# Optimization experiments

Measured on AMD Instinct MI355X. Metric: run time of the kernel, lower is better.

Reference implementation:

```python
import jax, jax.numpy as jnp
import numpy as np

EMB_DIM = 1024
N_HEADS = 16
HEAD_DIM = EMB_DIM // N_HEADS
WINDOW = 128
B, T = 4, 2048


def setup_inputs() -> dict:
    key = jax.random.key(0)
    k1, k2, k3 = jax.random.split(key, 3)
    x = jax.random.normal(k1, (B, T, EMB_DIM), dtype=jnp.float32)
    # nn.Linear weights: stored as [out, in], applied as x @ W^T
    s1 = 1.0 / np.sqrt(EMB_DIM)
    w_qkv = jax.random.uniform(k2, (3 * EMB_DIM, EMB_DIM), jnp.float32, -s1, s1)
    w_out = jax.random.uniform(k3, (EMB_DIM, EMB_DIM), jnp.float32, -s1, s1)
    return {"x": x, "w_qkv": w_qkv, "w_out": w_out}


def reference(x, w_qkv, w_out):
    Bs, Ts, C = x.shape
    scale = HEAD_DIM ** -0.5
    qkv = x @ w_qkv.T                                   # [B,T,3C]
    qkv = qkv.reshape(Bs, Ts, 3, N_HEADS, HEAD_DIM)
    qkv = jnp.transpose(qkv, (2, 0, 3, 1, 4))           # [3,B,H,T,D]
    q, k, v = qkv[0], qkv[1], qkv[2]
    scores = jnp.einsum('bhtd,bhsd->bhts', q, k) * scale  # [B,H,T,T]
    i = jnp.arange(Ts)[:, None]
    j = jnp.arange(Ts)[None, :]
    # causal AND within sliding window: i - WINDOW <= j <= i
    allowed = (j <= i) & (j >= i - WINDOW)               # [T,T] bool
    scores = jnp.where(allowed[None, None], scores, -jnp.inf)
    attn = jax.nn.softmax(scores, axis=-1)
    out = jnp.einsum('bhts,bhsd->bhtd', attn, v)         # [B,H,T,D]
    out = jnp.transpose(out, (0, 2, 1, 3)).reshape(Bs, Ts, C)
    return out @ w_out.T
```

## Files before the change

kernel.cpp:

```cpp
#include <hip/hip_runtime.h>
#include <hip/hip_bf16.h>
#include <stdint.h>

typedef __attribute__((ext_vector_type(8))) short bf16x8;
typedef __attribute__((ext_vector_type(4))) float f32x4;
typedef __attribute__((ext_vector_type(4))) unsigned short u16x4;

#define B_ 4
#define T_ 2048
#define C_ 1024
#define H_ 16
#define D_ 64

__device__ __forceinline__ unsigned short f2bf(float f) {
  union { float f; uint32_t u; } v; v.f = f;
  uint32_t u = v.u;
  uint32_t r = (u + 0x7FFFu + ((u >> 16) & 1u)) >> 16;
  return (unsigned short)r;
}

__global__ void __launch_bounds__(256) cast_all(const float* __restrict__ x,
                                                const float* __restrict__ wqkv,
                                                const float* __restrict__ wout,
                                                unsigned short* __restrict__ xb,
                                                unsigned short* __restrict__ wqkvb,
                                                unsigned short* __restrict__ woutb) {
  int bid = blockIdx.x;
  const float* src; unsigned short* dst; int i;
  if (bid < 8192)       { src = x;    dst = xb;    i = bid * 256 + threadIdx.x; }
  else if (bid < 11264) { src = wqkv; dst = wqkvb; i = (bid - 8192) * 256 + threadIdx.x; }
  else                  { src = wout; dst = woutb; i = (bid - 11264) * 256 + threadIdx.x; }
  float4 f = ((const float4*)src)[i];
  u16x4 o;
  o[0] = f2bf(f.x); o[1] = f2bf(f.y); o[2] = f2bf(f.z); o[3] = f2bf(f.w);
  ((u16x4*)dst)[i] = o;
}

__global__ void __launch_bounds__(256) gemm_qkv(const unsigned short* __restrict__ A,
                                                const unsigned short* __restrict__ Bm,
                                                unsigned short* __restrict__ qb,
                                                unsigned short* __restrict__ kb,
                                                unsigned short* __restrict__ vb) {
  __shared__ short lds[32768];
  const int tid = threadIdx.x;
  const int bm = blockIdx.y * 128;
  const int bn = blockIdx.x * 128;

  const int wave = tid >> 6;
  const int l = tid & 63;
  const int wm = wave >> 1, wn = wave & 1;
  const int lm = l & 15, lq = l >> 4;
  const int lr = l >> 2;
  const int lc = (l & 3) << 3;

  f32x4 acc[4][4];
#pragma unroll
  for (int i = 0; i < 4; i++)
#pragma unroll
    for (int j = 0; j < 4; j++) acc[i][j] = (f32x4){0.f, 0.f, 0.f, 0.f};

  const unsigned short* gsrc[4];
  int ldoff[4];
#pragma unroll
  for (int i = 0; i < 4; i++) {
    int c = wave * 4 + i;
    if (c < 8) {
      gsrc[i] = A + (size_t)(bm + 16 * c + lr) * 1024 + lc;
      ldoff[i] = c * 512;
    } else {
      gsrc[i] = Bm + (size_t)(bn + 16 * (c - 8) + lr) * 1024 + lc;
      ldoff[i] = 16384 + (c - 8) * 512;
    }
  }

#define STAGE(q, kk)                                                             \
  do {                                                                           \
    _Pragma("unroll")                                                            \
    for (int i = 0; i < 4; i++) {                                                \
      __builtin_amdgcn_global_load_lds(                                          \
          (__attribute__((address_space(1))) void*)(uintptr_t)(const void*)(gsrc[i] + (kk)), \
          (__attribute__((address_space(3))) void*)(lds + ldoff[i] + (q) * 4096),            \
          16, 0, 0);                                                             \
    }                                                                            \
  } while (0)

  STAGE(0, 0);
  STAGE(1, 32);
  __syncthreads();

  for (int kk = 0; kk < 1024; kk += 64) {
    const int cp = (kk >> 6) & 1;
    if (kk + 64 < 1024) {
      STAGE(2 * (1 - cp), kk + 64);
      STAGE(2 * (1 - cp) + 1, kk + 96);
    }
#pragma unroll
    for (int sub = 0; sub < 2; sub++) {
      const int q = 2 * cp + sub;
      const short* As_ = lds + q * 4096;
      const short* Bs_ = lds + 16384 + q * 4096;
      bf16x8 af[4], bfr[4];
#pragma unroll
      for (int i = 0; i < 4; i++)
        af[i] = *(const bf16x8*)&As_[(wm * 64 + 16 * i + lm) * 32 + 8 * lq];
#pragma unroll
      for (int j = 0; j < 4; j++)
        bfr[j] = *(const bf16x8*)&Bs_[(wn * 64 + 16 * j + lm) * 32 + 8 * lq];
#pragma unroll
      for (int i = 0; i < 4; i++)
#pragma unroll
        for (int j = 0; j < 4; j++)
          acc[i][j] = __builtin_amdgcn_mfma_f32_16x16x32_bf16(af[i], bfr[j], acc[i][j], 0, 0, 0);
    }
    __syncthreads();
  }
#undef STAGE

  if (bn >= 2048) {
#pragma unroll
    for (int i = 0; i < 4; i++)
#pragma unroll
      for (int j = 0; j < 4; j++) {
        int m0 = bm + wm * 64 + 16 * i + 4 * lq;
        int n = (bn - 2048) + wn * 64 + 16 * j + lm;
        int h = n >> 6, d = n & 63;
        int b = m0 >> 11, t = m0 & 2047;
        u16x4 o;
#pragma unroll
        for (int r = 0; r < 4; r++) o[r] = f2bf(acc[i][j][r]);
        *(u16x4*)&vb[(((size_t)(b * 16 + h)) * 64 + d) * 2048 + t] = o;
      }
  } else {
#pragma unroll
    for (int i = 0; i < 4; i++)
#pragma unroll
      for (int j = 0; j < 4; j++)
#pragma unroll
        for (int r = 0; r < 4; r++)
          lds[(wm * 64 + 16 * i + 4 * lq + r) * 132 + wn * 64 + 16 * j + lm] =
              (short)f2bf(acc[i][j][r]);
    __syncthreads();
#pragma unroll
    for (int k = 0; k < 8; k++) {
      int c = tid + 256 * k;
      int row = c >> 4;
      int col = (c & 15) << 3;
      bf16x8 v = *(const bf16x8*)&lds[row * 132 + col];
      int m = bm + row, n = bn + col;
      int which = n >> 10, rem = n & 1023;
      int h = rem >> 6, d = rem & 63;
      int b = m >> 11, t = m & 2047;
      unsigned short* dst = (which == 0) ? qb : kb;
      *(bf16x8*)&dst[(((size_t)(b * 16 + h)) * 2048 + t) * 64 + d] = v;
    }
  }
}

__global__ void __launch_bounds__(256) gemm_out(const unsigned short* __restrict__ A,
                                                const unsigned short* __restrict__ Bm,
                                                float* __restrict__ fo) {
  __shared__ short lds[32768];
  const int tid = threadIdx.x;
  const int bm = blockIdx.y * 128;
  const int bn = blockIdx.x * 128;
  const int wave = tid >> 6;
  const int l = tid & 63;
  const int wm = wave >> 1, wn = wave & 1;
  const int lm = l & 15, lq = l >> 4;
  const int lr = l >> 2;
  const int lc = (l & 3) << 3;

  f32x4 acc[4][4];
#pragma unroll
  for (int i = 0; i < 4; i++)
#pragma unroll
    for (int j = 0; j < 4; j++) acc[i][j] = (f32x4){0.f, 0.f, 0.f, 0.f};

  const unsigned short* gsrc[4];
  int ldoff[4];
#pragma unroll
  for (int i = 0; i < 4; i++) {
    int c = wave * 4 + i;
    if (c < 8) {
      gsrc[i] = A + (size_t)(bm + 16 * c + lr) * 1024 + lc;
      ldoff[i] = c * 512;
    } else {
      gsrc[i] = Bm + (size_t)(bn + 16 * (c - 8) + lr) * 1024 + lc;
      ldoff[i] = 16384 + (c - 8) * 512;
    }
  }

#define STAGE(q, kk)                                                             \
  do {                                                                           \
    _Pragma("unroll")                                                            \
    for (int i = 0; i < 4; i++) {                                                \
      __builtin_amdgcn_global_load_lds(                                          \
          (__attribute__((address_space(1))) void*)(uintptr_t)(const void*)(gsrc[i] + (kk)), \
          (__attribute__((address_space(3))) void*)(lds + ldoff[i] + (q) * 4096),            \
          16, 0, 0);                                                             \
    }                                                                            \
  } while (0)

  STAGE(0, 0);
  STAGE(1, 32);
  __syncthreads();

  for (int kk = 0; kk < 1024; kk += 64) {
    const int cp = (kk >> 6) & 1;
    if (kk + 64 < 1024) {
      STAGE(2 * (1 - cp), kk + 64);
      STAGE(2 * (1 - cp) + 1, kk + 96);
    }
#pragma unroll
    for (int sub = 0; sub < 2; sub++) {
      const int q = 2 * cp + sub;
      const short* As_ = lds + q * 4096;
      const short* Bs_ = lds + 16384 + q * 4096;
      bf16x8 af[4], bfr[4];
#pragma unroll
      for (int i = 0; i < 4; i++)
        af[i] = *(const bf16x8*)&As_[(wm * 64 + 16 * i + lm) * 32 + 8 * lq];
#pragma unroll
      for (int j = 0; j < 4; j++)
        bfr[j] = *(const bf16x8*)&Bs_[(wn * 64 + 16 * j + lm) * 32 + 8 * lq];
#pragma unroll
      for (int i = 0; i < 4; i++)
#pragma unroll
        for (int j = 0; j < 4; j++)
          acc[i][j] = __builtin_amdgcn_mfma_f32_16x16x32_bf16(af[i], bfr[j], acc[i][j], 0, 0, 0);
    }
    __syncthreads();
  }
#undef STAGE

#pragma unroll
  for (int i = 0; i < 4; i++)
#pragma unroll
    for (int j = 0; j < 4; j++)
#pragma unroll
      for (int r = 0; r < 4; r++) {
        int m = bm + wm * 64 + 16 * i + 4 * lq + r;
        int n = bn + wn * 64 + 16 * j + lm;
        fo[(size_t)m * 1024 + n] = acc[i][j][r];
      }
}

__global__ void __launch_bounds__(256, 4) attn_swa(const unsigned short* __restrict__ Qb,
                                                   const unsigned short* __restrict__ Kb,
                                                   const unsigned short* __restrict__ Vt,
                                                   unsigned short* __restrict__ Ob) {
  __shared__ short P[4][16 * 48];
  const int wv = threadIdx.x >> 6;
  const int l = threadIdx.x & 63;
  const int wid = blockIdx.x * 4 + wv;
  const int bh = wid >> 6;
  const int t0 = (wid & 63) << 5;
  const int lm = l & 15, lq = l >> 4;
  const size_t base = (size_t)bh * (T_ * D_);

  bf16x8 qf[2][2];
#pragma unroll
  for (int qt = 0; qt < 2; qt++) {
    qf[qt][0] = *(const bf16x8*)(Qb + base + (size_t)(t0 + 16 * qt + lm) * 64 + 8 * lq);
    qf[qt][1] = *(const bf16x8*)(Qb + base + (size_t)(t0 + 16 * qt + lm) * 64 + 32 + 8 * lq);
  }

  float mst[2] = {-1e30f, -1e30f}, lst[2] = {0.f, 0.f};
  f32x4 Oa[2][4];
#pragma unroll
  for (int qt = 0; qt < 2; qt++)
#pragma unroll
    for (int jt = 0; jt < 4; jt++) Oa[qt][jt] = (f32x4){0.f, 0.f, 0.f, 0.f};

  const float cs = 0.125f * 1.44269504f;
  int jstart = t0 - 128; if (jstart < 0) jstart = 0;

  for (int j0 = jstart; j0 < t0 + 32; j0 += 32) {
    bf16x8 ka[2][2];
#pragma unroll
    for (int hh = 0; hh < 2; hh++) {
      int kr = j0 + 16 * hh + lm;
      ka[hh][0] = *(const bf16x8*)(Kb + base + (size_t)kr * 64 + 8 * lq);
      ka[hh][1] = *(const bf16x8*)(Kb + base + (size_t)kr * 64 + 32 + 8 * lq);
    }
    bf16x8 vf[4];
#pragma unroll
    for (int jt = 0; jt < 4; jt++)
      vf[jt] = *(const bf16x8*)(Vt + base + (size_t)(16 * jt + lm) * 2048 + j0 + 8 * lq);

#pragma unroll
    for (int qt = 0; qt < 2; qt++) {
      const int t0q = t0 + 16 * qt;
      const int t = t0q + lm;
      f32x4 s0 = (f32x4){0.f, 0.f, 0.f, 0.f}, s1 = (f32x4){0.f, 0.f, 0.f, 0.f};
      s0 = __builtin_amdgcn_mfma_f32_16x16x32_bf16(ka[0][0], qf[qt][0], s0, 0, 0, 0);
      s0 = __builtin_amdgcn_mfma_f32_16x16x32_bf16(ka[0][1], qf[qt][1], s0, 0, 0, 0);
      s1 = __builtin_amdgcn_mfma_f32_16x16x32_bf16(ka[1][0], qf[qt][0], s1, 0, 0, 0);
      s1 = __builtin_amdgcn_mfma_f32_16x16x32_bf16(ka[1][1], qf[qt][1], s1, 0, 0, 0);
      float sv[8];
      float m2 = -1e30f;
#pragma unroll
      for (int hh = 0; hh < 2; hh++)
#pragma unroll
        for (int r = 0; r < 4; r++) {
          int k = j0 + 16 * hh + 4 * lq + r;
          float x = (hh ? s1[r] : s0[r]) * cs;
          bool okm = (k <= t) && (k + 128 >= t);
          sv[hh * 4 + r] = okm ? x : -1e30f;
          m2 = fmaxf(m2, sv[hh * 4 + r]);
        }
      m2 = fmaxf(m2, __shfl_xor(m2, 16));
      m2 = fmaxf(m2, __shfl_xor(m2, 32));
      float mn = fmaxf(mst[qt], m2);
      float a = __builtin_amdgcn_exp2f(mst[qt] - mn);
      float ps = 0.f;
#pragma unroll
      for (int i = 0; i < 8; i++) {
        sv[i] = (sv[i] > -1e29f) ? __builtin_amdgcn_exp2f(sv[i] - mn) : 0.f;
        ps += sv[i];
      }
      ps += __shfl_xor(ps, 16);
      ps += __shfl_xor(ps, 32);
      lst[qt] = lst[qt] * a + ps;
      mst[qt] = mn;
#pragma unroll
      for (int hh = 0; hh < 2; hh++) {
        u16x4 pk;
#pragma unroll
        for (int r = 0; r < 4; r++) pk[r] = f2bf(sv[hh * 4 + r]);
        *(u16x4*)&P[wv][lm * 48 + 16 * hh + 4 * lq] = pk;
      }
      float al[4];
#pragma unroll
      for (int r = 0; r < 4; r++) al[r] = __shfl(a, 4 * lq + r);
#pragma unroll
      for (int jt = 0; jt < 4; jt++)
#pragma unroll
        for (int r = 0; r < 4; r++) Oa[qt][jt][r] *= al[r];
      bf16x8 pa = *(const bf16x8*)&P[wv][lm * 48 + 8 * lq];
#pragma unroll
      for (int jt = 0; jt < 4; jt++)
        Oa[qt][jt] = __builtin_amdgcn_mfma_f32_16x16x32_bf16(pa, vf[jt], Oa[qt][jt], 0, 0, 0);
    }
  }
  const int b = bh >> 4, h = bh & 15;
#pragma unroll
  for (int qt = 0; qt < 2; qt++) {
    float inv = 1.0f / lst[qt];
    float invl[4];
#pragma unroll
    for (int r = 0; r < 4; r++) invl[r] = __shfl(inv, 4 * lq + r);
#pragma unroll
    for (int r = 0; r < 4; r++) {
      int t = t0 + 16 * qt + 4 * lq + r;
#pragma unroll
      for (int jt = 0; jt < 4; jt++) {
        int c = h * 64 + 16 * jt + lm;
        Ob[((size_t)(b * T_ + t)) * 1024 + c] = f2bf(Oa[qt][jt][r] * invl[r]);
      }
    }
  }
}

extern "C" void kernel_launch(void* const* d_in, const int* in_sizes, int n_in,
                              void* d_out, int out_size, void* d_ws, size_t ws_size,
                              hipStream_t stream) {
  const float* x = (const float*)d_in[0];
  const float* w_qkv = (const float*)d_in[1];
  const float* w_out = (const float*)d_in[2];
  float* out = (float*)d_out;

  unsigned short* xb = (unsigned short*)d_ws;
  unsigned short* wqkvb = xb + (size_t)8192 * 1024;
  unsigned short* woutb = wqkvb + (size_t)3072 * 1024;
  unsigned short* qb = woutb + (size_t)1024 * 1024;
  unsigned short* kb = qb + (size_t)64 * 2048 * 64;
  unsigned short* vb = kb + (size_t)64 * 2048 * 64;

  cast_all<<<12288, 256, 0, stream>>>(x, w_qkv, w_out, xb, wqkvb, woutb);

  gemm_qkv<<<dim3(24, 64), 256, 0, stream>>>(xb, wqkvb, qb, kb, vb);

  attn_swa<<<1024, 256, 0, stream>>>(qb, kb, vb, xb);

  gemm_out<<<dim3(8, 64), 256, 0, stream>>>(xb, woutb, out);
}
```

Baseline: 205.0 us.

## Specialize attention mask per KV block and skip lazy softmax rescales

Splits the sliding-window attention KV loop into first/interior/diagonal blocks with template-specialized masks, so interior blocks skip mask evaluation entirely. Adds a lazy-rescale path that keeps the old running max when the new block max is within a threshold, avoiding the output-accumulator rescale and its shuffles. Also swaps the manual bf16 rounding for the HIP intrinsic conversion. The lazy-max path depends on exp2 of bounded values staying in range and adds a wave vote and a branch per step; masked entries now rely on exp2 of a very negative number underflowing to zero.

```diff
diff --git a/kernel.cpp b/kernel.cpp
--- a/kernel.cpp
+++ b/kernel.cpp
@@ -17,6 +17,13 @@
   uint32_t u = v.u;
   uint32_t r = (u + 0x7FFFu + ((u >> 16) & 1u)) >> 16;
   return (unsigned short)r;
+}
+
+__device__ __forceinline__ unsigned short f2bfh(float f) {
+  __hip_bfloat16 h = __float2bfloat16(f);
+  unsigned short u;
+  __builtin_memcpy(&u, &h, 2);
+  return u;
 }
 
 __global__ void __launch_bounds__(256) cast_all(const float* __restrict__ x,
@@ -245,6 +252,73 @@
       }
 }
 
+template <int MODE>
+__device__ __forceinline__ void qt_step(int j0, int t0q, int lm, int lq, short* Pw,
+                                        const bf16x8 (&ka)[2][2], const bf16x8 (&vf)[4],
+                                        bf16x8 qf0, bf16x8 qf1,
+                                        float& mstq, float& lstq, f32x4 (&Oaq)[4]) {
+  const float cs = 0.125f * 1.44269504f;
+  const int t = t0q + lm;
+  f32x4 s0 = (f32x4){0.f, 0.f, 0.f, 0.f}, s1 = (f32x4){0.f, 0.f, 0.f, 0.f};
+  s0 = __builtin_amdgcn_mfma_f32_16x16x32_bf16(ka[0][0], qf0, s0, 0, 0, 0);
+  s0 = __builtin_amdgcn_mfma_f32_16x16x32_bf16(ka[0][1], qf1, s0, 0, 0, 0);
+  s1 = __builtin_amdgcn_mfma_f32_16x16x32_bf16(ka[1][0], qf0, s1, 0, 0, 0);
+  s1 = __builtin_amdgcn_mfma_f32_16x16x32_bf16(ka[1][1], qf1, s1, 0, 0, 0);
+  float sv[8];
+  float m2 = -1e30f;
+#pragma unroll
+  for (int hh = 0; hh < 2; hh++)
+#pragma unroll
+    for (int r = 0; r < 4; r++) {
+      int k = j0 + 16 * hh + 4 * lq + r;
+      float x = (hh ? s1[r] : s0[r]) * cs;
+      bool okm = (MODE == 2) ? true
+               : (MODE == 1) ? (k + 128 >= t)
+               : (MODE == 3) ? (k <= t)
+                             : ((k <= t) && (k + 128 >= t));
+      sv[hh * 4 + r] = okm ? x : -1e30f;
+      m2 = fmaxf(m2, sv[hh * 4 + r]);
+    }
+  m2 = fmaxf(m2, __shfl_xor(m2, 16));
+  m2 = fmaxf(m2, __shfl_xor(m2, 32));
+  if (__all(m2 <= mstq + 8.0f)) {
+    float ps = 0.f;
+#pragma unroll
+    for (int i = 0; i < 8; i++) { sv[i] = __builtin_amdgcn_exp2f(sv[i] - mstq); ps += sv[i]; }
+    ps += __shfl_xor(ps, 16);
+    ps += __shfl_xor(ps, 32);
+    lstq += ps;
+  } else {
+    float mn = fmaxf(mstq, m2);
+    float a = __builtin_amdgcn_exp2f(mstq - mn);
+    float ps = 0.f;
+#pragma unroll
+    for (int i = 0; i < 8; i++) { sv[i] = __builtin_amdgcn_exp2f(sv[i] - mn); ps += sv[i]; }
+    ps += __shfl_xor(ps, 16);
+    ps += __shfl_xor(ps, 32);
+    lstq = lstq * a + ps;
+    mstq = mn;
+    float al[4];
+#pragma unroll
+    for (int r = 0; r < 4; r++) al[r] = __shfl(a, 4 * lq + r);
+#pragma unroll
+    for (int jt = 0; jt < 4; jt++)
+#pragma unroll
+      for (int r = 0; r < 4; r++) Oaq[jt][r] *= al[r];
+  }
+#pragma unroll
+  for (int hh = 0; hh < 2; hh++) {
+    u16x4 pk;
+#pragma unroll
+    for (int r = 0; r < 4; r++) pk[r] = f2bfh(sv[hh * 4 + r]);
+    *(u16x4*)&Pw[lm * 48 + 16 * hh + 4 * lq] = pk;
+  }
+  bf16x8 pa = *(const bf16x8*)&Pw[lm * 48 + 8 * lq];
+#pragma unroll
+  for (int jt = 0; jt < 4; jt++)
+    Oaq[jt] = __builtin_amdgcn_mfma_f32_16x16x32_bf16(pa, vf[jt], Oaq[jt], 0, 0, 0);
+}
+
 __global__ void __launch_bounds__(256, 4) attn_swa(const unsigned short* __restrict__ Qb,
                                                    const unsigned short* __restrict__ Kb,
                                                    const unsigned short* __restrict__ Vt,
@@ -257,6 +331,7 @@
   const int t0 = (wid & 63) << 5;
   const int lm = l & 15, lq = l >> 4;
   const size_t base = (size_t)bh * (T_ * D_);
+  short* Pw = &P[wv][0];
 
   bf16x8 qf[2][2];
 #pragma unroll
@@ -272,77 +347,42 @@
 #pragma unroll
     for (int jt = 0; jt < 4; jt++) Oa[qt][jt] = (f32x4){0.f, 0.f, 0.f, 0.f};
 
-  const float cs = 0.125f * 1.44269504f;
-  int jstart = t0 - 128; if (jstart < 0) jstart = 0;
-
-  for (int j0 = jstart; j0 < t0 + 32; j0 += 32) {
-    bf16x8 ka[2][2];
-#pragma unroll
-    for (int hh = 0; hh < 2; hh++) {
-      int kr = j0 + 16 * hh + lm;
-      ka[hh][0] = *(const bf16x8*)(Kb + base + (size_t)kr * 64 + 8 * lq);
-      ka[hh][1] = *(const bf16x8*)(Kb + base + (size_t)kr * 64 + 32 + 8 * lq);
-    }
-    bf16x8 vf[4];
-#pragma unroll
-    for (int jt = 0; jt < 4; jt++)
-      vf[jt] = *(const bf16x8*)(Vt + base + (size_t)(16 * jt + lm) * 2048 + j0 + 8 * lq);
-
-#pragma unroll
-    for (int qt = 0; qt < 2; qt++) {
-      const int t0q = t0 + 16 * qt;
-      const int t = t0q + lm;
-      f32x4 s0 = (f32x4){0.f, 0.f, 0.f, 0.f}, s1 = (f32x4){0.f, 0.f, 0.f, 0.f};
-      s0 = __builtin_amdgcn_mfma_f32_16x16x32_bf16(ka[0][0], qf[qt][0], s0, 0, 0, 0);
-      s0 = __builtin_amdgcn_mfma_f32_16x16x32_bf16(ka[0][1], qf[qt][1], s0, 0, 0, 0);
-      s1 = __builtin_amdgcn_mfma_f32_16x16x32_bf16(ka[1][0], qf[qt][0], s1, 0, 0, 0);
-      s1 = __builtin_amdgcn_mfma_f32_16x16x32_bf16(ka[1][1], qf[qt][1], s1, 0, 0, 0);
-      float sv[8];
-      float m2 = -1e30f;
-#pragma unroll
-      for (int hh = 0; hh < 2; hh++)
-#pragma unroll
-        for (int r = 0; r < 4; r++) {
-          int k = j0 + 16 * hh + 4 * lq + r;
-          float x = (hh ? s1[r] : s0[r]) * cs;
-          bool okm = (k <= t) && (k + 128 >= t);
-          sv[hh * 4 + r] = okm ? x : -1e30f;
-          m2 = fmaxf(m2, sv[hh * 4 + r]);
-        }
-      m2 = fmaxf(m2, __shfl_xor(m2, 16));
-      m2 = fmaxf(m2, __shfl_xor(m2, 32));
-      float mn = fmaxf(mst[qt], m2);
-      float a = __builtin_amdgcn_exp2f(mst[qt] - mn);
-      float ps = 0.f;
-#pragma unroll
-      for (int i = 0; i < 8; i++) {
-        sv[i] = (sv[i] > -1e29f) ? __builtin_amdgcn_exp2f(sv[i] - mn) : 0.f;
-        ps += sv[i];
-      }
-      ps += __shfl_xor(ps, 16);
-      ps += __shfl_xor(ps, 32);
-      lst[qt] = lst[qt] * a + ps;
-      mst[qt] = mn;
-#pragma unroll
-      for (int hh = 0; hh < 2; hh++) {
-        u16x4 pk;
-#pragma unroll
-        for (int r = 0; r < 4; r++) pk[r] = f2bf(sv[hh * 4 + r]);
-        *(u16x4*)&P[wv][lm * 48 + 16 * hh + 4 * lq] = pk;
-      }
-      float al[4];
-#pragma unroll
-      for (int r = 0; r < 4; r++) al[r] = __shfl(a, 4 * lq + r);
-#pragma unroll
-      for (int jt = 0; jt < 4; jt++)
-#pragma unroll
-        for (int r = 0; r < 4; r++) Oa[qt][jt][r] *= al[r];
-      bf16x8 pa = *(const bf16x8*)&P[wv][lm * 48 + 8 * lq];
-#pragma unroll
-      for (int jt = 0; jt < 4; jt++)
-        Oa[qt][jt] = __builtin_amdgcn_mfma_f32_16x16x32_bf16(pa, vf[jt], Oa[qt][jt], 0, 0, 0);
-    }
-  }
+#define LOADKV(J0)                                                               \
+  bf16x8 ka[2][2];                                                               \
+  _Pragma("unroll")                                                              \
+  for (int hh = 0; hh < 2; hh++) {                                               \
+    int kr = (J0) + 16 * hh + lm;                                                \
+    ka[hh][0] = *(const bf16x8*)(Kb + base + (size_t)kr * 64 + 8 * lq);          \
+    ka[hh][1] = *(const bf16x8*)(Kb + base + (size_t)kr * 64 + 32 + 8 * lq);     \
+  }                                                                              \
+  bf16x8 vf[4];                                                                  \
+  _Pragma("unroll")                                                              \
+  for (int jt = 0; jt < 4; jt++)                                                 \
+    vf[jt] = *(const bf16x8*)(Vt + base + (size_t)(16 * jt + lm) * 2048 + (J0) + 8 * lq)
+
+  if (t0 >= 128) {
+    { LOADKV(t0 - 128);
+      qt_step<1>(t0 - 128, t0, lm, lq, Pw, ka, vf, qf[0][0], qf[0][1], mst[0], lst[0], Oa[0]);
+      qt_step<1>(t0 - 128, t0 + 16, lm, lq, Pw, ka, vf, qf[1][0], qf[1][1], mst[1], lst[1], Oa[1]); }
+#pragma unroll
+    for (int c = 1; c <= 3; c++) {
+      int j0 = t0 - 128 + 32 * c;
+      LOADKV(j0);
+      qt_step<2>(j0, t0, lm, lq, Pw, ka, vf, qf[0][0], qf[0][1], mst[0], lst[0], Oa[0]);
+      qt_step<2>(j0, t0 + 16, lm, lq, Pw, ka, vf, qf[1][0], qf[1][1], mst[1], lst[1], Oa[1]);
+    }
+    { LOADKV(t0);
+      qt_step<3>(t0, t0, lm, lq, Pw, ka, vf, qf[0][0], qf[0][1], mst[0], lst[0], Oa[0]);
+      qt_step<3>(t0, t0 + 16, lm, lq, Pw, ka, vf, qf[1][0], qf[1][1], mst[1], lst[1], Oa[1]); }
+  } else {
+    for (int j0 = 0; j0 < t0 + 32; j0 += 32) {
+      LOADKV(j0);
+      qt_step<3>(j0, t0, lm, lq, Pw, ka, vf, qf[0][0], qf[0][1], mst[0], lst[0], Oa[0]);
+      qt_step<3>(j0, t0 + 16, lm, lq, Pw, ka, vf, qf[1][0], qf[1][1], mst[1], lst[1], Oa[1]);
+    }
+  }
+#undef LOADKV
+
   const int b = bh >> 4, h = bh & 15;
 #pragma unroll
   for (int qt = 0; qt < 2; qt++) {
@@ -356,7 +396,7 @@
 #pragma unroll
       for (int jt = 0; jt < 4; jt++) {
         int c = h * 64 + 16 * jt + lm;
-        Ob[((size_t)(b * T_ + t)) * 1024 + c] = f2bf(Oa[qt][jt][r] * invl[r]);
+        Ob[((size_t)(b * T_ + t)) * 1024 + c] = f2bfh(Oa[qt][jt][r] * invl[r]);
       }
     }
   }
```

Result: slower. 233.9 us (+14.1%).
